# Kernel tuning notes

Hardware: AMD Instinct MI355X
Metric: run time of the kernel (lower is better)

## Reference

```python
import jax, jax.numpy as jnp
import numpy as np

B, L = 2, 2048
D_MODEL, D_INNER, D_STATE, DT_RANK, D_CONV, DEPTH = 1024, 2048, 16, 64, 4, 2
EPS = 1e-5


def setup_inputs() -> dict:
    key = jax.random.key(0)
    ks = jax.random.split(key, 8)
    rn = lambda k, s, scale=0.02: jax.random.normal(k, s, jnp.float32) * scale
    return {
        "x": jax.random.normal(ks[0], (B, L, D_MODEL), jnp.float32),
        "x_size": L,  # truthiness flag only; unused in the math
        "norm_w": jnp.ones((DEPTH, D_MODEL), jnp.float32),
        "norm_b": jnp.zeros((DEPTH, D_MODEL), jnp.float32),
        "in_proj_w": rn(ks[1], (DEPTH, 2 * D_INNER, D_MODEL)),
        "conv_w": rn(ks[2], (DEPTH, D_INNER, 1, D_CONV), 0.1),
        "conv_b": jnp.zeros((DEPTH, D_INNER), jnp.float32),
        "x_proj_w": rn(ks[3], (DEPTH, DT_RANK + 2 * D_STATE, D_INNER)),
        "dt_proj_w": rn(ks[4], (DEPTH, D_INNER, DT_RANK), 0.1),
        "dt_proj_b": jnp.full((DEPTH, D_INNER), -4.0, jnp.float32),  # softplus -> small dt
        "A_log": jnp.broadcast_to(
            jnp.log(jnp.arange(1, D_STATE + 1, dtype=jnp.float32)), (DEPTH, D_INNER, D_STATE)
        ) + jnp.zeros((DEPTH, D_INNER, D_STATE), jnp.float32),
        "D": jnp.ones((DEPTH, D_INNER), jnp.float32),
        "out_proj_w": rn(ks[5], (DEPTH, D_MODEL, D_INNER)),
    }


def _layernorm(x, w, b):
    mu = x.mean(-1, keepdims=True)
    var = ((x - mu) ** 2).mean(-1, keepdims=True)
    return (x - mu) * jax.lax.rsqrt(var + EPS) * w + b


def _selective_scan(u, dt, A, Bm, Cm, Dp):
    # u, dt: (B, L, di); A: (di, n); Bm, Cm: (B, L, n); Dp: (di,)
    def step(h, inp):
        u_t, dt_t, B_t, C_t = inp  # (B,di), (B,di), (B,n), (B,n)
        dA = jnp.exp(dt_t[..., None] * A)                       # (B, di, n)
        h = dA * h + (dt_t * u_t)[..., None] * B_t[:, None, :]  # (B, di, n)
        y = jnp.einsum('bdn,bn->bd', h, C_t)
        return h, y

    h0 = jnp.zeros((u.shape[0], A.shape[0], A.shape[1]), u.dtype)
    xs = (u.swapaxes(0, 1), dt.swapaxes(0, 1), Bm.swapaxes(0, 1), Cm.swapaxes(0, 1))
    _, ys = jax.lax.scan(step, h0, xs)  # ys: (L, B, di)
    return ys.swapaxes(0, 1) + u * Dp


def _mamba(x, in_proj_w, conv_w, conv_b, x_proj_w, dt_proj_w, dt_proj_b, A_log, Dp, out_proj_w):
    xz = jnp.einsum('bld,ed->ble', x, in_proj_w)  # (B, L, 2*di)
    u, z = jnp.split(xz, 2, axis=-1)
    # causal depthwise conv1d, kernel D_CONV
    uc = jax.lax.conv_general_dilated(
        u.swapaxes(1, 2), conv_w, (1,), [(D_CONV - 1, 0)],
        feature_group_count=D_INNER, dimension_numbers=('NCH', 'OIH', 'NCH'))
    u = jax.nn.silu(uc.swapaxes(1, 2) + conv_b)
    x_dbl = jnp.einsum('bld,ed->ble', u, x_proj_w)
    dt_r, Bm, Cm = jnp.split(x_dbl, [DT_RANK, DT_RANK + D_STATE], axis=-1)
    dt = jax.nn.softplus(jnp.einsum('blr,dr->bld', dt_r, dt_proj_w) + dt_proj_b)
    A = -jnp.exp(A_log)
    y = _selective_scan(u, dt, A, Bm, Cm, Dp)
    y = y * jax.nn.silu(z)
    return jnp.einsum('bld,ed->ble', y, out_proj_w)


def reference(x, x_size, norm_w, norm_b, in_proj_w, conv_w, conv_b, x_proj_w,
              dt_proj_w, dt_proj_b, A_log, D, out_proj_w):
    # BasicLayer passes x_size as `residual` (non-None), so each Block reduces to
    # x <- Mamba(LN(x)); the returned residual is discarded by x = blk(...)[0].
    h = x
    for i in range(DEPTH):
        hn = _layernorm(h, norm_w[i], norm_b[i])
        h = _mamba(hn, in_proj_w[i], conv_w[i], conv_b[i], x_proj_w[i],
                   dt_proj_w[i], dt_proj_b[i], A_log[i], D[i], out_proj_w[i])
    return h
```

## Files before the change

### kernel.cpp

```cpp
#include <hip/hip_runtime.h>
#include <hip/hip_bf16.h>
#include <math.h>

#define BQ 2
#define LQ 2048
#define D_MODEL 1024
#define D_INNER 2048
#define D_STATE 16
#define DT_RANK 64
#define D_CONV 4
#define DEPTH 2
#define NCHUNK 64
#define CHUNK 32
#define XSPLITK 8
#define XKC (D_INNER / XSPLITK)
#define OSK 2

typedef __attribute__((ext_vector_type(8))) short short8v;
typedef __attribute__((ext_vector_type(4))) float f32x4;

__device__ __forceinline__ short f2bf(float f) {
    union { float f; unsigned u; } v; v.f = f;
    unsigned r = v.u + 0x7fffu + ((v.u >> 16) & 1u);
    return (short)(r >> 16);
}

__device__ __forceinline__ float bf2f(unsigned short s) {
    union { unsigned u; float f; } v; v.u = ((unsigned)s) << 16;
    return v.f;
}

__device__ __forceinline__ void async16(void* lds, const void* gp) {
    __builtin_amdgcn_global_load_lds(
        (const __attribute__((address_space(1))) void*)gp,
        (__attribute__((address_space(3))) void*)lds, 16, 0, 0);
}

__device__ __forceinline__ void dA_powers(float e1, float* dA) {
    float e2 = e1 * e1, e4 = e2 * e2, e8 = e4 * e4;
    dA[0] = e1;       dA[1] = e2;       dA[2] = e2 * e1;  dA[3] = e4;
    dA[4] = e4 * e1;  dA[5] = e4 * e2;  dA[6] = e4 * dA[2]; dA[7] = e8;
    dA[8] = e8 * e1;  dA[9] = e8 * e2;  dA[10] = e8 * dA[2]; dA[11] = e8 * e4;
    dA[12] = e8 * dA[4]; dA[13] = e8 * dA[5]; dA[14] = e8 * dA[6]; dA[15] = e8 * e8;
}

__global__ __launch_bounds__(256) void layernorm_kernel(
    const float* __restrict__ x, const float* __restrict__ w,
    const float* __restrict__ b, short* __restrict__ out)
{
    __shared__ float red[8];
    int row = blockIdx.x;
    const float* xr = x + (size_t)row * D_MODEL;
    float v[4];
    float s = 0.f, sq = 0.f;
#pragma unroll
    for (int i = 0; i < 4; ++i) {
        v[i] = xr[threadIdx.x + i * 256];
        s += v[i];
        sq += v[i] * v[i];
    }
#pragma unroll
    for (int off = 32; off; off >>= 1) {
        s += __shfl_down(s, off, 64);
        sq += __shfl_down(sq, off, 64);
    }
    int wid = threadIdx.x >> 6, lane = threadIdx.x & 63;
    if (!lane) { red[wid] = s; red[4 + wid] = sq; }
    __syncthreads();
    s = red[0] + red[1] + red[2] + red[3];
    sq = red[4] + red[5] + red[6] + red[7];
    float mu = s * (1.f / D_MODEL);
    float var = sq * (1.f / D_MODEL) - mu * mu;
    float rstd = rsqrtf(var + 1e-5f);
#pragma unroll
    for (int i = 0; i < 4; ++i) {
        int c = threadIdx.x + i * 256;
        out[(size_t)row * D_MODEL + c] = f2bf((v[i] - mu) * rstd * w[c] + b[c]);
    }
}

__global__ __launch_bounds__(256) void osum_ln_kernel(
    const float* __restrict__ P, const float* __restrict__ w,
    const float* __restrict__ b, short* __restrict__ out)
{
    __shared__ float red[8];
    int row = blockIdx.x;
    const float* p0 = P + (size_t)row * D_MODEL;
    const float* p1 = P + (size_t)BQ * LQ * D_MODEL + (size_t)row * D_MODEL;
    float v[4];
    float s = 0.f, sq = 0.f;
#pragma unroll
    for (int i = 0; i < 4; ++i) {
        int c = threadIdx.x + i * 256;
        v[i] = p0[c] + p1[c];
        s += v[i];
        sq += v[i] * v[i];
    }
#pragma unroll
    for (int off = 32; off; off >>= 1) {
        s += __shfl_down(s, off, 64);
        sq += __shfl_down(sq, off, 64);
    }
    int wid = threadIdx.x >> 6, lane = threadIdx.x & 63;
    if (!lane) { red[wid] = s; red[4 + wid] = sq; }
    __syncthreads();
    s = red[0] + red[1] + red[2] + red[3];
    sq = red[4] + red[5] + red[6] + red[7];
    float mu = s * (1.f / D_MODEL);
    float var = sq * (1.f / D_MODEL) - mu * mu;
    float rstd = rsqrtf(var + 1e-5f);
#pragma unroll
    for (int i = 0; i < 4; ++i) {
        int c = threadIdx.x + i * 256;
        out[(size_t)row * D_MODEL + c] = f2bf((v[i] - mu) * rstd * w[c] + b[c]);
    }
}

__global__ __launch_bounds__(512) void gemm256_bf16_kernel(
    const short* __restrict__ A, const short* __restrict__ W,
    short* __restrict__ C, int M, int N, int K)
{
    __shared__ __align__(16) short lds[65536];
    const int tid = threadIdx.x;
    const int lane = tid & 63;
    const int w = tid >> 6;
    const int wr = w >> 2, wc = w & 3;

    int nbx = N >> 8;
    int nwg = (M >> 8) * nbx;
    int q = nwg >> 3;
    int wg = ((int)blockIdx.x & 7) * q + ((int)blockIdx.x >> 3);
    int bx = wg % nbx, by = wg / nbx;
    int bm = by << 8, bn = bx << 8;

    const int fr = lane & 15;
    const int kl = lane >> 4;
    const int srow = lane >> 3;
    const int schunk = (lane & 7) ^ (srow & 7);

    f32x4 acc[8][4] = {};
    short8v af[4][2], bfA[2][2], bfB[2][2];

    auto STAGE = [&](int isA, int buf, int half, int kt) {
        const short* gp = isA ? A : W;
        int tile0 = isA ? bm : bn;
        int base = (isA ? 0 : 32768) + (buf * 2 + half) * 8192;
        int ko = kt << 6;
#pragma unroll
        for (int s = 0; s < 2; ++s) {
            int row = half * 128 + s * 64 + w * 8 + srow;
            const short* src = gp + (size_t)(tile0 + row) * K + ko + schunk * 8;
            async16(&lds[base + s * 4096 + w * 512], src);
        }
    };

    auto LOAD_A = [&](int buf, int mh) {
        int abase = (buf * 2 + mh) * 8192;
#pragma unroll
        for (int i = 0; i < 4; ++i) {
            int rl = wr * 64 + i * 16 + fr;
            int rsw = rl & 7;
#pragma unroll
            for (int ks = 0; ks < 2; ++ks)
                af[i][ks] = *(const short8v*)&lds[abase + rl * 64 + (((ks * 4 + kl) ^ rsw) * 8)];
        }
    };
    auto LOAD_B = [&](int buf, int nh, short8v (&bf)[2][2]) {
        int bbase = 32768 + (buf * 2 + nh) * 8192;
#pragma unroll
        for (int j = 0; j < 2; ++j) {
            int rl = wc * 32 + j * 16 + fr;
            int rsw = rl & 7;
#pragma unroll
            for (int ks = 0; ks < 2; ++ks)
                bf[j][ks] = *(const short8v*)&lds[bbase + rl * 64 + (((ks * 4 + kl) ^ rsw) * 8)];
        }
    };
    auto MFMA_Q = [&](int mh, int nh, short8v (&bf)[2][2]) {
        __builtin_amdgcn_s_setprio(1);
#pragma unroll
        for (int i = 0; i < 4; ++i)
#pragma unroll
            for (int j = 0; j < 2; ++j)
#pragma unroll
                for (int ks = 0; ks < 2; ++ks)
                    acc[mh * 4 + i][nh * 2 + j] = __builtin_amdgcn_mfma_f32_16x16x32_bf16(
                        af[i][ks], bf[j][ks], acc[mh * 4 + i][nh * 2 + j], 0, 0, 0);
        __builtin_amdgcn_s_setprio(0);
    };

#define GBAR  __builtin_amdgcn_s_barrier(); __builtin_amdgcn_sched_barrier(0);
#define LGKM  asm volatile("s_waitcnt lgkmcnt(0)" ::: "memory"); __builtin_amdgcn_sched_barrier(0);

    STAGE(1, 0, 0, 0); STAGE(0, 0, 0, 0);
    STAGE(1, 0, 1, 0); STAGE(0, 0, 1, 0);
    STAGE(1, 1, 0, 1); STAGE(0, 1, 0, 1);

    int T = K >> 7;
    for (int t = 0; t < T; ++t) {
        int last = (t == T - 1);
        asm volatile("s_waitcnt vmcnt(4)" ::: "memory");
        STAGE(1, 1, 1, 2 * t + 1);
        GBAR;
        LOAD_A(0, 0); LOAD_B(0, 0, bfA);
        LGKM; MFMA_Q(0, 0, bfA);
        GBAR;
        STAGE(0, 1, 1, 2 * t + 1);
        GBAR;
        LOAD_B(0, 1, bfB);
        LGKM; MFMA_Q(0, 1, bfB);
        GBAR;
        if (!last) STAGE(1, 0, 0, 2 * t + 2);
        GBAR;
        LOAD_A(0, 1);
        LGKM; MFMA_Q(1, 1, bfB);
        GBAR;
        if (!last) STAGE(0, 0, 0, 2 * t + 2);
        GBAR;
        MFMA_Q(1, 0, bfA);
        GBAR;
        if (last) { asm volatile("s_waitcnt vmcnt(0)" ::: "memory"); }
        else      { asm volatile("s_waitcnt vmcnt(4)" ::: "memory"); }
        if (!last) STAGE(1, 0, 1, 2 * t + 2);
        GBAR;
        LOAD_A(1, 0); LOAD_B(1, 0, bfA);
        LGKM; MFMA_Q(0, 0, bfA);
        GBAR;
        if (!last) STAGE(0, 0, 1, 2 * t + 2);
        GBAR;
        LOAD_B(1, 1, bfB);
        LGKM; MFMA_Q(0, 1, bfB);
        GBAR;
        if (!last) STAGE(1, 1, 0, 2 * t + 3);
        GBAR;
        LOAD_A(1, 1);
        LGKM; MFMA_Q(1, 1, bfB);
        GBAR;
        if (!last) STAGE(0, 1, 0, 2 * t + 3);
        GBAR;
        MFMA_Q(1, 0, bfA);
        GBAR;
    }
#undef GBAR
#undef LGKM

    int cr = (lane >> 4) * 4, cc = lane & 15;
#pragma unroll
    for (int i8 = 0; i8 < 8; ++i8) {
        int mh = i8 >> 2, ii = i8 & 3;
        int row0 = bm + mh * 128 + wr * 64 + ii * 16 + cr;
#pragma unroll
        for (int p = 0; p < 4; ++p) {
            short* Cp = C + (size_t)(row0 + p) * N + bn;
#pragma unroll
            for (int j4 = 0; j4 < 4; ++j4) {
                int nh = j4 >> 1, jj = j4 & 1;
                Cp[nh * 128 + wc * 32 + jj * 16 + cc] = f2bf(acc[i8][j4][p]);
            }
        }
    }
}

__global__ __launch_bounds__(256) void gemm_bf16_kernel(
    const short* __restrict__ A, const short* __restrict__ W,
    void* __restrict__ Cv, int M, int N, int K,
    const float* __restrict__ bias, int epilogue, int nsk)
{
    __shared__ __align__(16) short As[2][128 * 64];
    __shared__ __align__(16) short Bs[2][128 * 64];
    int tid = threadIdx.x;
    int lane = tid & 63, wv = tid >> 6;
    int nbx = N >> 7;
    int nwg = (M >> 7) * nbx;
    int ntot = nwg * nsk;
    int q = ntot >> 3;
    int wgz = ((int)blockIdx.x & 7) * q + ((int)blockIdx.x >> 3);
    int sk = wgz / nwg;
    int wg = wgz % nwg;
    int bx = wg % nbx, by = wg / nbx;
    int bm = by * 128, bn = bx * 128;
    int wr = wv >> 1, wc = wv & 1;
    int Kl = K / nsk;
    int koff = sk * Kl;

    const int fr = lane & 15;
    const int kl = lane >> 4;
    const int srow = lane >> 3;
    const int schunk = (lane & 7) ^ (srow & 7);

    f32x4 acc[4][4] = {};

    const short* Ab = A + (size_t)bm * K + koff;
    const short* Bb = W + (size_t)bn * K + koff;

    auto STAGE = [&](int buf, int kt) {
        int ko = kt << 6;
#pragma unroll
        for (int s = 0; s < 4; ++s) {
            int row = s * 32 + wv * 8 + srow;
            async16(&As[buf][s * 2048 + wv * 512], Ab + (size_t)row * K + ko + schunk * 8);
            async16(&Bs[buf][s * 2048 + wv * 512], Bb + (size_t)row * K + ko + schunk * 8);
        }
    };

    int NT = Kl >> 6;
    STAGE(0, 0);
    if (NT > 1) STAGE(1, 1);

    for (int t = 0; t < NT; ++t) {
        if (t + 1 < NT) { asm volatile("s_waitcnt vmcnt(8)" ::: "memory"); }
        else            { asm volatile("s_waitcnt vmcnt(0)" ::: "memory"); }
        __builtin_amdgcn_s_barrier();
        __builtin_amdgcn_sched_barrier(0);
        int buf = t & 1;
        short8v af[4][2], bf[4][2];
#pragma unroll
        for (int i = 0; i < 4; ++i) {
            int rl = wr * 64 + i * 16 + fr;
            int rsw = rl & 7;
#pragma unroll
            for (int ks = 0; ks < 2; ++ks)
                af[i][ks] = *(const short8v*)&As[buf][rl * 64 + (((ks * 4 + kl) ^ rsw) * 8)];
        }
#pragma unroll
        for (int j = 0; j < 4; ++j) {
            int rl = wc * 64 + j * 16 + fr;
            int rsw = rl & 7;
#pragma unroll
            for (int ks = 0; ks < 2; ++ks)
                bf[j][ks] = *(const short8v*)&Bs[buf][rl * 64 + (((ks * 4 + kl) ^ rsw) * 8)];
        }
        asm volatile("s_waitcnt lgkmcnt(0)" ::: "memory");
        __builtin_amdgcn_sched_barrier(0);
        __builtin_amdgcn_s_setprio(1);
#pragma unroll
        for (int i = 0; i < 4; ++i)
#pragma unroll
            for (int j = 0; j < 4; ++j)
#pragma unroll
                for (int ks = 0; ks < 2; ++ks)
                    acc[i][j] = __builtin_amdgcn_mfma_f32_16x16x32_bf16(
                        af[i][ks], bf[j][ks], acc[i][j], 0, 0, 0);
        __builtin_amdgcn_s_setprio(0);
        __builtin_amdgcn_s_barrier();
        __builtin_amdgcn_sched_barrier(0);
        if (t + 2 < NT) STAGE(buf, t + 2);
    }

    int cr = (lane >> 4) * 4, cc = lane & 15;
    size_t skoff = (size_t)sk * M * N;
#pragma unroll
    for (int i = 0; i < 4; ++i)
#pragma unroll
        for (int p = 0; p < 4; ++p) {
            int row = bm + wr * 64 + i * 16 + cr + p;
#pragma unroll
            for (int j = 0; j < 4; ++j) {
                int col = bn + wc * 64 + cc + j * 16;
                float v = acc[i][j][p];
                if (epilogue == 2)
                    ((short*)Cv)[(size_t)row * N + col] = f2bf(v);
                else
                    ((float*)Cv)[skoff + (size_t)row * N + col] = v;
            }
        }
}

__global__ __launch_bounds__(256) void osum_kernel(
    const float* __restrict__ P, float* __restrict__ out)
{
    size_t i = ((size_t)blockIdx.x * 256 + threadIdx.x) * 4;
    float4 a = *(const float4*)(P + i);
    float4 b = *(const float4*)(P + (size_t)BQ * LQ * D_MODEL + i);
    a.x += b.x; a.y += b.y; a.z += b.z; a.w += b.w;
    *(float4*)(out + i) = a;
}

__global__ __launch_bounds__(256) void dtproj_kernel(
    const short* __restrict__ A, const short* __restrict__ W,
    const float* __restrict__ bias, short* __restrict__ Out)
{
    int lane = threadIdx.x & 63, w = threadIdx.x >> 6;
    int m0 = blockIdx.y * 64 + w * 16;
    int bn = blockIdx.x * 128;
    int fr = lane & 15, fk = (lane >> 4) * 8;
    const short* Ap = A + (size_t)(m0 + fr) * DT_RANK + fk;
    short8v a0 = *(const short8v*)(Ap);
    short8v a1 = *(const short8v*)(Ap + 32);
    f32x4 acc[8] = {};
#pragma unroll
    for (int j = 0; j < 8; ++j) {
        const short* Wp = W + (size_t)(bn + j * 16 + fr) * DT_RANK + fk;
        short8v b0 = *(const short8v*)(Wp);
        short8v b1 = *(const short8v*)(Wp + 32);
        acc[j] = __builtin_amdgcn_mfma_f32_16x16x32_bf16(a0, b0, acc[j], 0, 0, 0);
        acc[j] = __builtin_amdgcn_mfma_f32_16x16x32_bf16(a1, b1, acc[j], 0, 0, 0);
    }
    int cr = (lane >> 4) * 4, cc = lane & 15;
#pragma unroll
    for (int j = 0; j < 8; ++j) {
        int col = bn + j * 16 + cc;
        float bv = bias[col];
#pragma unroll
        for (int p = 0; p < 4; ++p) {
            float v = acc[j][p] + bv;
            v = (v > 20.f) ? v : __logf(1.f + __expf(v));
            Out[(size_t)(m0 + cr + p) * D_INNER + col] = f2bf(v);
        }
    }
}

__global__ __launch_bounds__(256) void xproj_kernel(
    const short* __restrict__ A, const short* __restrict__ W,
    float* __restrict__ Xpart)
{
    int lane = threadIdx.x & 63, wv = threadIdx.x >> 6;
    int sk = blockIdx.x;
    int m0 = blockIdx.y * 64 + wv * 16;
    int fr = lane & 15, fk = (lane >> 4) * 8;
    const short* Ap = A + (size_t)(m0 + fr) * D_INNER + sk * XKC + fk;
    const short* Wp = W + (size_t)fr * D_INNER + sk * XKC + fk;
    f32x4 acc[6] = {};
    for (int k = 0; k < XKC; k += 32) {
        short8v af = *(const short8v*)(Ap + k);
#pragma unroll
        for (int j = 0; j < 6; ++j) {
            short8v bf = *(const short8v*)(Wp + (size_t)j * 16 * D_INNER + k);
            acc[j] = __builtin_amdgcn_mfma_f32_16x16x32_bf16(af, bf, acc[j], 0, 0, 0);
        }
    }
    int cr = (lane >> 4) * 4, cc = lane & 15;
    float* Op = Xpart + ((size_t)sk * (BQ * LQ) + m0 + cr) * 96 + cc;
#pragma unroll
    for (int j = 0; j < 6; ++j)
#pragma unroll
        for (int p = 0; p < 4; ++p)
            Op[(size_t)p * 96 + j * 16] = acc[j][p];
}

__global__ __launch_bounds__(256) void xreduce_kernel(
    const float* __restrict__ Xpart, float* __restrict__ xdbl,
    short* __restrict__ dtr)
{
    size_t i = (size_t)blockIdx.x * 256 + threadIdx.x;
    float s = 0.f;
#pragma unroll
    for (int sk = 0; sk < XSPLITK; ++sk)
        s += Xpart[(size_t)sk * ((size_t)BQ * LQ * 96) + i];
    xdbl[i] = s;
    int col = (int)(i % 96);
    if (col < DT_RANK)
        dtr[(i / 96) * DT_RANK + col] = f2bf(s);
}

__global__ __launch_bounds__(256) void conv_silu_kernel(
    const unsigned short* __restrict__ uz, short* __restrict__ outb,
    const float* __restrict__ w, const float* __restrict__ bias)
{
    int idx = blockIdx.x * 256 + threadIdx.x;
    int e0 = idx * 2;
    int c = e0 & (D_INNER - 1);
    int bl = e0 / D_INNER;
    int l = bl & (LQ - 1);
    int b = bl / LQ;
    float acc0 = bias[c], acc1 = bias[c + 1];
    float w0[D_CONV], w1[D_CONV];
#pragma unroll
    for (int k = 0; k < D_CONV; ++k) {
        w0[k] = w[c * D_CONV + k];
        w1[k] = w[(c + 1) * D_CONV + k];
    }
#pragma unroll
    for (int k = 0; k < D_CONV; ++k) {
        int ls = l - (D_CONV - 1) + k;
        if (ls >= 0) {
            unsigned v = *(const unsigned*)&uz[((size_t)b * LQ + ls) * (2 * D_INNER) + c];
            acc0 += bf2f((unsigned short)(v & 0xffff)) * w0[k];
            acc1 += bf2f((unsigned short)(v >> 16)) * w1[k];
        }
    }
    float v0 = acc0 / (1.f + __expf(-acc0));
    float v1 = acc1 / (1.f + __expf(-acc1));
    unsigned o = (unsigned)(unsigned short)f2bf(v0) |
                 ((unsigned)(unsigned short)f2bf(v1) << 16);
    *(unsigned*)&outb[e0] = o;
}

__global__ __launch_bounds__(256) void scan_phase1_kernel(
    const unsigned short* __restrict__ u, const unsigned short* __restrict__ dt,
    const float* __restrict__ xdbl, const float* __restrict__ A_log,
    float* __restrict__ dtsumb, float* __restrict__ Fbuf)
{
    __shared__ float S[CHUNK][D_STATE];
    __shared__ __align__(16) unsigned short Ub[2][8][256];
    __shared__ __align__(16) unsigned short Db[2][8][256];
    int t = threadIdx.x;
    int d0 = blockIdx.x * 256;
    int d = d0 + t;
    int c = blockIdx.y;
    int b = blockIdx.z;
    int l0 = c * CHUNK;
    {
        int row = t >> 3, cc2 = (t & 7) * 2;
        const float* src = xdbl + ((size_t)(b * LQ + l0 + row)) * 96 + DT_RANK + cc2;
        *(float2*)&S[row][cc2] = *(const float2*)src;
    }
    const int w = t >> 6, lane = t & 63;
    const int srw = 2 * w + (lane >> 5);
    const int scl = (lane & 31) * 8;
    const unsigned short* ubp = u  + ((size_t)b * LQ + l0) * D_INNER + d0;
    const unsigned short* dbp = dt + ((size_t)b * LQ + l0) * D_INNER + d0;
    auto STAGE1 = [&](int buf, int lb) {
        async16(&Ub[buf][2 * w][0], ubp + (size_t)(lb + srw) * D_INNER + scl);
        async16(&Db[buf][2 * w][0], dbp + (size_t)(lb + srw) * D_INNER + scl);
    };
    STAGE1(0, 0);

    float A[D_STATE], h[D_STATE];
    {
        const float4* ap = (const float4*)(A_log + (size_t)d * D_STATE);
#pragma unroll
        for (int g = 0; g < 4; ++g) {
            float4 a = ap[g];
            A[g*4+0] = -__expf(a.x); A[g*4+1] = -__expf(a.y);
            A[g*4+2] = -__expf(a.z); A[g*4+3] = -__expf(a.w);
        }
    }
    bool pf = true;
#pragma unroll
    for (int n = 1; n < D_STATE; ++n)
        pf = pf && (fabsf(A[n] - (float)(n + 1) * A[0]) <= 1e-4f * (float)(n + 1));
#pragma unroll
    for (int n = 0; n < D_STATE; ++n) h[n] = 0.f;
    float dtsum = 0.f;
    float A0 = A[0];
    asm volatile("s_waitcnt lgkmcnt(0)" ::: "memory");

    for (int bb = 0; bb < CHUNK / 8; ++bb) {
        int buf = bb & 1;
        if (bb + 1 < CHUNK / 8) {
            STAGE1(buf ^ 1, (bb + 1) * 8);
            asm volatile("s_waitcnt vmcnt(2)" ::: "memory");
        } else {
            asm volatile("s_waitcnt vmcnt(0)" ::: "memory");
        }
        __builtin_amdgcn_s_barrier();
        __builtin_amdgcn_sched_barrier(0);
        float uvv[8], dtvv[8];
#pragma unroll
        for (int i = 0; i < 8; ++i) {
            uvv[i]  = bf2f(Ub[buf][i][t]);
            dtvv[i] = bf2f(Db[buf][i][t]);
        }
        if (pf) {
#pragma unroll
            for (int i = 0; i < 8; ++i) {
                int l = bb * 8 + i;
                float dtv = dtvv[i];
                float du = dtv * uvv[i];
                dtsum += dtv;
                float dA[D_STATE];
                dA_powers(__expf(dtv * A0), dA);
#pragma unroll
                for (int n4 = 0; n4 < D_STATE; n4 += 4) {
                    float4 Bv = *(const float4*)&S[l][n4];
                    float bb2[4] = {Bv.x, Bv.y, Bv.z, Bv.w};
#pragma unroll
                    for (int k = 0; k < 4; ++k) {
                        int n = n4 + k;
                        h[n] = dA[n] * h[n] + du * bb2[k];
                    }
                }
            }
        } else {
#pragma unroll
            for (int i = 0; i < 8; ++i) {
                int l = bb * 8 + i;
                float dtv = dtvv[i];
                float du = dtv * uvv[i];
                dtsum += dtv;
#pragma unroll
                for (int n4 = 0; n4 < D_STATE; n4 += 4) {
                    float4 Bv = *(const float4*)&S[l][n4];
                    float bb2[4] = {Bv.x, Bv.y, Bv.z, Bv.w};
#pragma unroll
                    for (int k = 0; k < 4; ++k) {
                        int n = n4 + k;
                        float dA = __expf(dtv * A[n]);
                        h[n] = dA * h[n] + du * bb2[k];
                    }
                }
            }
        }
        __builtin_amdgcn_s_barrier();
        __builtin_amdgcn_sched_barrier(0);
    }
    dtsumb[(size_t)(b * NCHUNK + c) * D_INNER + d] = dtsum;
    size_t base = ((size_t)(b * NCHUNK + c) * D_STATE) * D_INNER + d;
#pragma unroll
    for (int n = 0; n < D_STATE; ++n)
        Fbuf[base + (size_t)n * D_INNER] = h[n];
}

__global__ __launch_bounds__(256) void scan_phase2_kernel(
    const float* __restrict__ dtsumb, const float* __restrict__ A_log,
    float* __restrict__ Fbuf)
{
    int d = blockIdx.x * 256 + threadIdx.x;
    int n = blockIdx.y;
    int b = blockIdx.z;
    float A = -__expf(A_log[(size_t)d * D_STATE + n]);
    float hinit = 0.f;
    for (int c = 0; c < NCHUNK; ++c) {
        size_t idx = ((size_t)(b * NCHUNK + c) * D_STATE + n) * D_INNER + d;
        float F = Fbuf[idx];
        float P = __expf(A * dtsumb[(size_t)(b * NCHUNK + c) * D_INNER + d]);
        Fbuf[idx] = hinit;
        hinit = P * hinit + F;
    }
}

__global__ __launch_bounds__(256) void scan_phase3_kernel(
    const unsigned short* __restrict__ u, const unsigned short* __restrict__ dt,
    const float* __restrict__ xdbl, const float* __restrict__ A_log,
    const float* __restrict__ Dp, const float* __restrict__ Hinit,
    const unsigned short* __restrict__ uz, short* __restrict__ yout)
{
    __shared__ float S[CHUNK][32];
    __shared__ __align__(16) unsigned short Ub[2][8][256];
    __shared__ __align__(16) unsigned short Db[2][8][256];
    __shared__ __align__(16) unsigned short Zb[2][8][256];
    int t = threadIdx.x;
    int d0 = blockIdx.x * 256;
    int d = d0 + t;
    int c = blockIdx.y;
    int b = blockIdx.z;
    int l0 = c * CHUNK;
    {
        int row = t >> 3, cg = (t & 7) * 4;
        const float* src = xdbl + ((size_t)(b * LQ + l0 + row)) * 96 + DT_RANK + cg;
        *(float4*)&S[row][cg ^ ((row & 7) << 2)] = *(const float4*)src;
    }
    const int w = t >> 6, lane = t & 63;
    const int srw = 2 * w + (lane >> 5);
    const int scl = (lane & 31) * 8;
    const unsigned short* ubp = u  + ((size_t)b * LQ + l0) * D_INNER + d0;
    const unsigned short* dbp = dt + ((size_t)b * LQ + l0) * D_INNER + d0;
    const unsigned short* zbp = uz + ((size_t)b * LQ + l0) * (2 * D_INNER) + D_INNER + d0;
    auto STAGE3 = [&](int buf, int lb) {
        async16(&Ub[buf][2 * w][0], ubp + (size_t)(lb + srw) * D_INNER + scl);
        async16(&Db[buf][2 * w][0], dbp + (size_t)(lb + srw) * D_INNER + scl);
        async16(&Zb[buf][2 * w][0], zbp + (size_t)(lb + srw) * (2 * D_INNER) + scl);
    };
    STAGE3(0, 0);

    float A[D_STATE], h[D_STATE];
    {
        const float4* ap = (const float4*)(A_log + (size_t)d * D_STATE);
#pragma unroll
        for (int g = 0; g < 4; ++g) {
            float4 a = ap[g];
            A[g*4+0] = -__expf(a.x); A[g*4+1] = -__expf(a.y);
            A[g*4+2] = -__expf(a.z); A[g*4+3] = -__expf(a.w);
        }
    }
    bool pf = true;
#pragma unroll
    for (int n = 1; n < D_STATE; ++n)
        pf = pf && (fabsf(A[n] - (float)(n + 1) * A[0]) <= 1e-4f * (float)(n + 1));
    size_t base = ((size_t)(b * NCHUNK + c) * D_STATE) * D_INNER + d;
#pragma unroll
    for (int n = 0; n < D_STATE; ++n)
        h[n] = Hinit[base + (size_t)n * D_INNER];
    float Dd = Dp[d];
    float A0 = A[0];
    short* yp = yout + ((size_t)b * LQ + l0) * D_INNER + d;
    asm volatile("s_waitcnt lgkmcnt(0)" ::: "memory");

    for (int bb = 0; bb < CHUNK / 8; ++bb) {
        int buf = bb & 1;
        if (bb + 1 < CHUNK / 8) {
            STAGE3(buf ^ 1, (bb + 1) * 8);
            asm volatile("s_waitcnt vmcnt(3)" ::: "memory");
        } else {
            asm volatile("s_waitcnt vmcnt(0)" ::: "memory");
        }
        __builtin_amdgcn_s_barrier();
        __builtin_amdgcn_sched_barrier(0);
        float uvv[8], dtvv[8], zvv[8];
#pragma unroll
        for (int i = 0; i < 8; ++i) {
            uvv[i]  = bf2f(Ub[buf][i][t]);
            dtvv[i] = bf2f(Db[buf][i][t]);
            zvv[i]  = bf2f(Zb[buf][i][t]);
        }
        if (pf) {
#pragma unroll
            for (int i = 0; i < 8; ++i) {
                int l = bb * 8 + i;
                float dtv = dtvv[i];
                float du = dtv * uvv[i];
                float acc = 0.f;
                int sw = (l & 7) << 2;
                float dA[D_STATE];
                dA_powers(__expf(dtv * A0), dA);
#pragma unroll
                for (int n4 = 0; n4 < D_STATE; n4 += 4) {
                    float4 Bv = *(const float4*)&S[l][n4 ^ sw];
                    float4 Cv = *(const float4*)&S[l][(16 + n4) ^ sw];
                    float bb2[4] = {Bv.x, Bv.y, Bv.z, Bv.w};
                    float cc2[4] = {Cv.x, Cv.y, Cv.z, Cv.w};
#pragma unroll
                    for (int k = 0; k < 4; ++k) {
                        int n = n4 + k;
                        h[n] = dA[n] * h[n] + du * bb2[k];
                        acc += h[n] * cc2[k];
                    }
                }
                float y = acc + uvv[i] * Dd;
                float zv = zvv[i];
                float g = zv / (1.f + __expf(-zv));
                yp[(size_t)l * D_INNER] = f2bf(y * g);
            }
        } else {
#pragma unroll
            for (int i = 0; i < 8; ++i) {
                int l = bb * 8 + i;
                float dtv = dtvv[i];
                float du = dtv * uvv[i];
                float acc = 0.f;
                int sw = (l & 7) << 2;
#pragma unroll
                for (int n4 = 0; n4 < D_STATE; n4 += 4) {
                    float4 Bv = *(const float4*)&S[l][n4 ^ sw];
                    float4 Cv = *(const float4*)&S[l][(16 + n4) ^ sw];
                    float bb2[4] = {Bv.x, Bv.y, Bv.z, Bv.w};
                    float cc2[4] = {Cv.x, Cv.y, Cv.z, Cv.w};
#pragma unroll
                    for (int k = 0; k < 4; ++k) {
                        int n = n4 + k;
                        float dA = __expf(dtv * A[n]);
                        h[n] = dA * h[n] + du * bb2[k];
                        acc += h[n] * cc2[k];
                    }
                }
                float y = acc + uvv[i] * Dd;
                float zv = zvv[i];
                float g = zv / (1.f + __expf(-zv));
                yp[(size_t)l * D_INNER] = f2bf(y * g);
            }
        }
        __builtin_amdgcn_s_barrier();
        __builtin_amdgcn_sched_barrier(0);
    }
}

__global__ __launch_bounds__(256) void convert_all_kernel(
    const float* __restrict__ w_in, const float* __restrict__ w_out,
    const float* __restrict__ w_xp, const float* __restrict__ w_dt,
    short* __restrict__ wbuf)
{
    const int IN_B  = (2 * D_INNER * D_MODEL) / 1024;
    const int OUT_B = (D_MODEL * D_INNER) / 1024;
    const int XP_B  = (96 * D_INNER) / 1024;
    int blk = blockIdx.x;
    const float* src; short* dst;
    if (blk < IN_B)                 { src = w_in;  dst = wbuf; }
    else if (blk < IN_B + OUT_B)    { src = w_out; dst = wbuf + 2 * D_INNER * D_MODEL; blk -= IN_B; }
    else if (blk < IN_B + OUT_B + XP_B) { src = w_xp; dst = wbuf + 2 * D_INNER * D_MODEL + D_MODEL * D_INNER; blk -= IN_B + OUT_B; }
    else { src = w_dt; dst = wbuf + 2 * D_INNER * D_MODEL + D_MODEL * D_INNER + 96 * D_INNER; blk -= IN_B + OUT_B + XP_B; }
    int i = blk * 1024 + threadIdx.x * 4;
    float4 v = *(const float4*)(src + i);
    short4 o = make_short4(f2bf(v.x), f2bf(v.y), f2bf(v.z), f2bf(v.w));
    *(short4*)(dst + i) = o;
}

extern "C" void kernel_launch(void* const* d_in, const int* in_sizes, int n_in,
                              void* d_out, int out_size, void* d_ws, size_t ws_size,
                              hipStream_t stream)
{
    const float* x        = (const float*)d_in[0];
    const float* norm_w   = (const float*)d_in[2];
    const float* norm_b   = (const float*)d_in[3];
    const float* in_proj  = (const float*)d_in[4];
    const float* conv_w   = (const float*)d_in[5];
    const float* conv_b   = (const float*)d_in[6];
    const float* x_proj   = (const float*)d_in[7];
    const float* dt_proj  = (const float*)d_in[8];
    const float* dt_projb = (const float*)d_in[9];
    const float* A_log    = (const float*)d_in[10];
    const float* Dp       = (const float*)d_in[11];
    const float* out_proj = (const float*)d_in[12];
    float* out = (float*)d_out;
    float* ws  = (float*)d_ws;

    const size_t BL   = (size_t)BQ * LQ;
    const size_t BLDM = BL * D_MODEL;
    const size_t BLDI = BL * D_INNER;
    const int IN_W  = 2 * D_INNER * D_MODEL;
    const int OUT_W = D_MODEL * D_INNER;
    const int XP_W  = 96 * D_INNER;
    const int DT_W  = D_INNER * DT_RANK;
    const int CV_BLOCKS = (IN_W + OUT_W + XP_W + DT_W) / 1024;

    size_t o = 0;
    short* hnb   = (short*)(ws + o); o += BLDM / 2;
    short* uzb   = (short*)(ws + o); o += BL * 2 * D_INNER / 2;
    short* dtb   = (short*)(ws + o); o += BLDI / 2;
    float* xdbl  = ws + o; o += BL * 96;
    float* Xpart = ws + o; o += (size_t)XSPLITK * BL * 96;
    float* Fbuf  = ws + o; o += (size_t)BQ * NCHUNK * D_STATE * D_INNER;
    float* dtsumb = ws + o; o += (size_t)BQ * NCHUNK * D_INNER;
    short* ucx   = (short*)(ws + o); o += BLDI / 2;
    short* dtr   = (short*)(ws + o); o += BL * DT_RANK / 2;
    float* Opart = ws + o; o += (size_t)OSK * BLDM;
    short* wbuf  = (short*)(ws + o);
    o += (size_t)(IN_W + OUT_W + XP_W + DT_W + 1) / 2;

    for (int layer = 0; layer < DEPTH; ++layer) {
        if (layer == 0)
            layernorm_kernel<<<(int)BL, 256, 0, stream>>>(
                x, norm_w, norm_b, hnb);

        convert_all_kernel<<<CV_BLOCKS, 256, 0, stream>>>(
            in_proj + (size_t)layer * IN_W, out_proj + (size_t)layer * OUT_W,
            x_proj + (size_t)layer * XP_W, dt_proj + (size_t)layer * DT_W, wbuf);

        gemm256_bf16_kernel<<<(int)(BL / 256) * (2 * D_INNER / 256), 512, 0, stream>>>(
            hnb, wbuf, uzb, (int)BL, 2 * D_INNER, D_MODEL);

        conv_silu_kernel<<<(int)(BLDI / 512), 256, 0, stream>>>(
            (const unsigned short*)uzb, ucx,
            conv_w + (size_t)layer * D_INNER * D_CONV,
            conv_b + (size_t)layer * D_INNER);

        xproj_kernel<<<dim3(XSPLITK, BL / 64), 256, 0, stream>>>(
            ucx, wbuf + IN_W + OUT_W, Xpart);
        xreduce_kernel<<<(int)(BL * 96 / 256), 256, 0, stream>>>(Xpart, xdbl, dtr);

        dtproj_kernel<<<dim3(D_INNER / 128, BL / 64), 256, 0, stream>>>(
            dtr, wbuf + IN_W + OUT_W + XP_W,
            dt_projb + (size_t)layer * D_INNER, dtb);

        const float* Al = A_log + (size_t)layer * D_INNER * D_STATE;
        scan_phase1_kernel<<<dim3(D_INNER / 256, NCHUNK, BQ), 256, 0, stream>>>(
            (const unsigned short*)ucx, (const unsigned short*)dtb, xdbl, Al,
            dtsumb, Fbuf);
        scan_phase2_kernel<<<dim3(D_INNER / 256, D_STATE, BQ), 256, 0, stream>>>(
            dtsumb, Al, Fbuf);
        scan_phase3_kernel<<<dim3(D_INNER / 256, NCHUNK, BQ), 256, 0, stream>>>(
            (const unsigned short*)ucx, (const unsigned short*)dtb, xdbl, Al,
            Dp + (size_t)layer * D_INNER, Fbuf,
            (const unsigned short*)uzb, (short*)ucx);

        gemm_bf16_kernel<<<(int)(BL / 128) * (D_MODEL / 128) * OSK, 256, 0, stream>>>(
            ucx, wbuf + IN_W, Opart, (int)BL, D_MODEL, D_INNER, nullptr, 0, OSK);

        if (layer == DEPTH - 1)
            osum_kernel<<<(int)(BLDM / 1024), 256, 0, stream>>>(Opart, out);
        else
            osum_ln_kernel<<<(int)BL, 256, 0, stream>>>(
                Opart, norm_w + (size_t)(layer + 1) * D_MODEL,
                norm_b + (size_t)(layer + 1) * D_MODEL, hnb);
    }
}
```

Measured before the change: 402.7 us.

## Simplify in_proj GEMM to double-buffered loop and store scan chunk states in bf16

Replaces the finely interleaved 8-phase in_proj GEMM schedule with a plain double-buffered loop: each iteration stages the full next K tile, then loads all fragments and issues all MFMAs, with each wave computing a 128x64 block. Separately, the scan's per-chunk carry buffer is stored as bf16 instead of fp32 to halve its memory traffic across the three scan phases. The GEMM change trades fine-grained load/compute overlap for fewer barriers and may raise register pressure; the bf16 carry states lose precision in the inter-chunk recurrence.

```diff
diff --git a/kernel.cpp b/kernel.cpp
--- a/kernel.cpp
+++ b/kernel.cpp
@@ -116,11 +116,12 @@
     }
 }
 
-__global__ __launch_bounds__(512) void gemm256_bf16_kernel(
+__global__ __launch_bounds__(512) void gemm256p2_kernel(
     const short* __restrict__ A, const short* __restrict__ W,
     short* __restrict__ C, int M, int N, int K)
 {
-    __shared__ __align__(16) short lds[65536];
+    __shared__ __align__(16) short As[2][256 * 64];
+    __shared__ __align__(16) short Bs[2][256 * 64];
     const int tid = threadIdx.x;
     const int lane = tid & 63;
     const int w = tid >> 6;
@@ -135,128 +136,82 @@
 
     const int fr = lane & 15;
     const int kl = lane >> 4;
-    const int srow = lane >> 3;
-    const int schunk = (lane & 7) ^ (srow & 7);
+    const int lrow = lane >> 3;
+    const int lchunk = (lane & 7) ^ (lrow & 7);
 
     f32x4 acc[8][4] = {};
-    short8v af[4][2], bfA[2][2], bfB[2][2];
-
-    auto STAGE = [&](int isA, int buf, int half, int kt) {
-        const short* gp = isA ? A : W;
-        int tile0 = isA ? bm : bn;
-        int base = (isA ? 0 : 32768) + (buf * 2 + half) * 8192;
+
+    const short* Ab = A + (size_t)bm * K;
+    const short* Bb = W + (size_t)bn * K;
+
+    auto STAGE = [&](int buf, int kt) {
         int ko = kt << 6;
 #pragma unroll
-        for (int s = 0; s < 2; ++s) {
-            int row = half * 128 + s * 64 + w * 8 + srow;
-            const short* src = gp + (size_t)(tile0 + row) * K + ko + schunk * 8;
-            async16(&lds[base + s * 4096 + w * 512], src);
+        for (int s = 0; s < 4; ++s) {
+            int row = s * 64 + w * 8 + lrow;
+            async16(&As[buf][(s * 64 + w * 8) * 64],
+                    Ab + (size_t)row * K + ko + lchunk * 8);
+            async16(&Bs[buf][(s * 64 + w * 8) * 64],
+                    Bb + (size_t)row * K + ko + lchunk * 8);
         }
     };
 
-    auto LOAD_A = [&](int buf, int mh) {
-        int abase = (buf * 2 + mh) * 8192;
-#pragma unroll
-        for (int i = 0; i < 4; ++i) {
-            int rl = wr * 64 + i * 16 + fr;
+    int NT = K >> 6;
+    STAGE(0, 0);
+
+    for (int t = 0; t < NT; ++t) {
+        if (t + 1 < NT) {
+            STAGE((t + 1) & 1, t + 1);
+            asm volatile("s_waitcnt vmcnt(8)" ::: "memory");
+        } else {
+            asm volatile("s_waitcnt vmcnt(0)" ::: "memory");
+        }
+        __builtin_amdgcn_s_barrier();
+        __builtin_amdgcn_sched_barrier(0);
+        int buf = t & 1;
+        short8v af[8][2], bf[4][2];
+#pragma unroll
+        for (int i = 0; i < 8; ++i) {
+            int rl = wr * 128 + i * 16 + fr;
             int rsw = rl & 7;
 #pragma unroll
             for (int ks = 0; ks < 2; ++ks)
-                af[i][ks] = *(const short8v*)&lds[abase + rl * 64 + (((ks * 4 + kl) ^ rsw) * 8)];
-        }
-    };
-    auto LOAD_B = [&](int buf, int nh, short8v (&bf)[2][2]) {
-        int bbase = 32768 + (buf * 2 + nh) * 8192;
-#pragma unroll
-        for (int j = 0; j < 2; ++j) {
-            int rl = wc * 32 + j * 16 + fr;
+                af[i][ks] = *(const short8v*)&As[buf][rl * 64 + (((ks * 4 + kl) ^ rsw) * 8)];
+        }
+#pragma unroll
+        for (int j = 0; j < 4; ++j) {
+            int rl = wc * 64 + j * 16 + fr;
             int rsw = rl & 7;
 #pragma unroll
             for (int ks = 0; ks < 2; ++ks)
-                bf[j][ks] = *(const short8v*)&lds[bbase + rl * 64 + (((ks * 4 + kl) ^ rsw) * 8)];
-        }
-    };
-    auto MFMA_Q = [&](int mh, int nh, short8v (&bf)[2][2]) {
+                bf[j][ks] = *(const short8v*)&Bs[buf][rl * 64 + (((ks * 4 + kl) ^ rsw) * 8)];
+        }
+        asm volatile("s_waitcnt lgkmcnt(0)" ::: "memory");
+        __builtin_amdgcn_sched_barrier(0);
         __builtin_amdgcn_s_setprio(1);
 #pragma unroll
-        for (int i = 0; i < 4; ++i)
-#pragma unroll
-            for (int j = 0; j < 2; ++j)
+        for (int i = 0; i < 8; ++i)
+#pragma unroll
+            for (int j = 0; j < 4; ++j)
 #pragma unroll
                 for (int ks = 0; ks < 2; ++ks)
-                    acc[mh * 4 + i][nh * 2 + j] = __builtin_amdgcn_mfma_f32_16x16x32_bf16(
-                        af[i][ks], bf[j][ks], acc[mh * 4 + i][nh * 2 + j], 0, 0, 0);
+                    acc[i][j] = __builtin_amdgcn_mfma_f32_16x16x32_bf16(
+                        af[i][ks], bf[j][ks], acc[i][j], 0, 0, 0);
         __builtin_amdgcn_s_setprio(0);
-    };
-
-#define GBAR  __builtin_amdgcn_s_barrier(); __builtin_amdgcn_sched_barrier(0);
-#define LGKM  asm volatile("s_waitcnt lgkmcnt(0)" ::: "memory"); __builtin_amdgcn_sched_barrier(0);
-
-    STAGE(1, 0, 0, 0); STAGE(0, 0, 0, 0);
-    STAGE(1, 0, 1, 0); STAGE(0, 0, 1, 0);
-    STAGE(1, 1, 0, 1); STAGE(0, 1, 0, 1);
-
-    int T = K >> 7;
-    for (int t = 0; t < T; ++t) {
-        int last = (t == T - 1);
-        asm volatile("s_waitcnt vmcnt(4)" ::: "memory");
-        STAGE(1, 1, 1, 2 * t + 1);
-        GBAR;
-        LOAD_A(0, 0); LOAD_B(0, 0, bfA);
-        LGKM; MFMA_Q(0, 0, bfA);
-        GBAR;
-        STAGE(0, 1, 1, 2 * t + 1);
-        GBAR;
-        LOAD_B(0, 1, bfB);
-        LGKM; MFMA_Q(0, 1, bfB);
-        GBAR;
-        if (!last) STAGE(1, 0, 0, 2 * t + 2);
-        GBAR;
-        LOAD_A(0, 1);
-        LGKM; MFMA_Q(1, 1, bfB);
-        GBAR;
-        if (!last) STAGE(0, 0, 0, 2 * t + 2);
-        GBAR;
-        MFMA_Q(1, 0, bfA);
-        GBAR;
-        if (last) { asm volatile("s_waitcnt vmcnt(0)" ::: "memory"); }
-        else      { asm volatile("s_waitcnt vmcnt(4)" ::: "memory"); }
-        if (!last) STAGE(1, 0, 1, 2 * t + 2);
-        GBAR;
-        LOAD_A(1, 0); LOAD_B(1, 0, bfA);
-        LGKM; MFMA_Q(0, 0, bfA);
-        GBAR;
-        if (!last) STAGE(0, 0, 1, 2 * t + 2);
-        GBAR;
-        LOAD_B(1, 1, bfB);
-        LGKM; MFMA_Q(0, 1, bfB);
-        GBAR;
-        if (!last) STAGE(1, 1, 0, 2 * t + 3);
-        GBAR;
-        LOAD_A(1, 1);
-        LGKM; MFMA_Q(1, 1, bfB);
-        GBAR;
-        if (!last) STAGE(0, 1, 0, 2 * t + 3);
-        GBAR;
-        MFMA_Q(1, 0, bfA);
-        GBAR;
-    }
-#undef GBAR
-#undef LGKM
+        __builtin_amdgcn_s_barrier();
+        __builtin_amdgcn_sched_barrier(0);
+    }
 
     int cr = (lane >> 4) * 4, cc = lane & 15;
 #pragma unroll
-    for (int i8 = 0; i8 < 8; ++i8) {
-        int mh = i8 >> 2, ii = i8 & 3;
-        int row0 = bm + mh * 128 + wr * 64 + ii * 16 + cr;
+    for (int i = 0; i < 8; ++i) {
+        int row0 = bm + wr * 128 + i * 16 + cr;
 #pragma unroll
         for (int p = 0; p < 4; ++p) {
-            short* Cp = C + (size_t)(row0 + p) * N + bn;
-#pragma unroll
-            for (int j4 = 0; j4 < 4; ++j4) {
-                int nh = j4 >> 1, jj = j4 & 1;
-                Cp[nh * 128 + wc * 32 + jj * 16 + cc] = f2bf(acc[i8][j4][p]);
-            }
+            short* Cp = C + (size_t)(row0 + p) * N + bn + wc * 64 + cc;
+#pragma unroll
+            for (int j = 0; j < 4; ++j)
+                Cp[j * 16] = f2bf(acc[i][j][p]);
         }
     }
 }
@@ -489,7 +444,7 @@
 __global__ __launch_bounds__(256) void scan_phase1_kernel(
     const unsigned short* __restrict__ u, const unsigned short* __restrict__ dt,
     const float* __restrict__ xdbl, const float* __restrict__ A_log,
-    float* __restrict__ dtsumb, float* __restrict__ Fbuf)
+    float* __restrict__ dtsumb, short* __restrict__ Fbuf)
 {
     __shared__ float S[CHUNK][D_STATE];
     __shared__ __align__(16) unsigned short Ub[2][8][256];
@@ -599,12 +554,12 @@
     size_t base = ((size_t)(b * NCHUNK + c) * D_STATE) * D_INNER + d;
 #pragma unroll
     for (int n = 0; n < D_STATE; ++n)
-        Fbuf[base + (size_t)n * D_INNER] = h[n];
+        Fbuf[base + (size_t)n * D_INNER] = f2bf(h[n]);
 }
 
 __global__ __launch_bounds__(256) void scan_phase2_kernel(
     const float* __restrict__ dtsumb, const float* __restrict__ A_log,
-    float* __restrict__ Fbuf)
+    short* __restrict__ Fbuf)
 {
     int d = blockIdx.x * 256 + threadIdx.x;
     int n = blockIdx.y;
@@ -613,9 +568,9 @@
     float hinit = 0.f;
     for (int c = 0; c < NCHUNK; ++c) {
         size_t idx = ((size_t)(b * NCHUNK + c) * D_STATE + n) * D_INNER + d;
-        float F = Fbuf[idx];
+        float F = bf2f(((const unsigned short*)Fbuf)[idx]);
         float P = __expf(A * dtsumb[(size_t)(b * NCHUNK + c) * D_INNER + d]);
-        Fbuf[idx] = hinit;
+        Fbuf[idx] = f2bf(hinit);
         hinit = P * hinit + F;
     }
 }
@@ -623,7 +578,7 @@
 __global__ __launch_bounds__(256) void scan_phase3_kernel(
     const unsigned short* __restrict__ u, const unsigned short* __restrict__ dt,
     const float* __restrict__ xdbl, const float* __restrict__ A_log,
-    const float* __restrict__ Dp, const float* __restrict__ Hinit,
+    const float* __restrict__ Dp, const unsigned short* __restrict__ Hinit,
     const unsigned short* __restrict__ uz, short* __restrict__ yout)
 {
     __shared__ float S[CHUNK][32];
@@ -671,7 +626,7 @@
     size_t base = ((size_t)(b * NCHUNK + c) * D_STATE) * D_INNER + d;
 #pragma unroll
     for (int n = 0; n < D_STATE; ++n)
-        h[n] = Hinit[base + (size_t)n * D_INNER];
+        h[n] = bf2f(Hinit[base + (size_t)n * D_INNER]);
     float Dd = Dp[d];
     float A0 = A[0];
     short* yp = yout + ((size_t)b * LQ + l0) * D_INNER + d;
@@ -809,7 +764,7 @@
     short* dtb   = (short*)(ws + o); o += BLDI / 2;
     float* xdbl  = ws + o; o += BL * 96;
     float* Xpart = ws + o; o += (size_t)XSPLITK * BL * 96;
-    float* Fbuf  = ws + o; o += (size_t)BQ * NCHUNK * D_STATE * D_INNER;
+    short* Fbuf  = (short*)(ws + o); o += (size_t)BQ * NCHUNK * D_STATE * D_INNER / 2;
     float* dtsumb = ws + o; o += (size_t)BQ * NCHUNK * D_INNER;
     short* ucx   = (short*)(ws + o); o += BLDI / 2;
     short* dtr   = (short*)(ws + o); o += BL * DT_RANK / 2;
@@ -826,7 +781,7 @@
             in_proj + (size_t)layer * IN_W, out_proj + (size_t)layer * OUT_W,
             x_proj + (size_t)layer * XP_W, dt_proj + (size_t)layer * DT_W, wbuf);
 
-        gemm256_bf16_kernel<<<(int)(BL / 256) * (2 * D_INNER / 256), 512, 0, stream>>>(
+        gemm256p2_kernel<<<(int)(BL / 256) * (2 * D_INNER / 256), 512, 0, stream>>>(
             hnb, wbuf, uzb, (int)BL, 2 * D_INNER, D_MODEL);
 
         conv_silu_kernel<<<(int)(BLDI / 512), 256, 0, stream>>>(
@@ -850,7 +805,7 @@
             dtsumb, Al, Fbuf);
         scan_phase3_kernel<<<dim3(D_INNER / 256, NCHUNK, BQ), 256, 0, stream>>>(
             (const unsigned short*)ucx, (const unsigned short*)dtb, xdbl, Al,
-            Dp + (size_t)layer * D_INNER, Fbuf,
+            Dp + (size_t)layer * D_INNER, (const unsigned short*)Fbuf,
             (const unsigned short*)uzb, (short*)ucx);
 
         gemm_bf16_kernel<<<(int)(BL / 128) * (D_MODEL / 128) * OSK, 256, 0, stream>>>(
```

After: 411.0 us. 1.02x slower.
